# Performance work log

Hardware: AMD Instinct MI355X
Metric: run time of the kernel (lower is better)

The kernel has to match this reference:

```python
import jax, jax.numpy as jnp
import numpy as np

B, S, E, H, D, W = 2, 4096, 512, 8, 64, 512
NUM_BUCKETS, MAX_DISTANCE = 32, 128  # hardcoded in get_relative_positions for 't5'
NEG_INF = -1e30


def _t5_bucket_causal(relative_position):
    """T5 relative position bucketing, unidirectional (causal)."""
    n = jnp.maximum(-relative_position, 0)
    max_exact = NUM_BUCKETS // 2
    is_small = n < max_exact
    nf = jnp.maximum(n.astype(jnp.float32), 1.0)
    val_if_large = max_exact + (
        jnp.log(nf / max_exact) / np.log(MAX_DISTANCE / max_exact)
        * (NUM_BUCKETS - max_exact)
    ).astype(jnp.int32)
    val_if_large = jnp.minimum(val_if_large, NUM_BUCKETS - 1)
    return jnp.where(is_small, n, val_if_large)


def setup_inputs() -> dict:
    key = jax.random.key(0)
    ks = jax.random.split(key, 7)
    scale = 1.0 / np.sqrt(E)  # keep logits in a sane range
    return {
        'xs': jax.random.normal(ks[0], (B, S, E), jnp.float32),
        'prev_k': jax.random.normal(ks[1], (B, W, H, D), jnp.float32),
        'prev_v': jax.random.normal(ks[2], (B, W, H, D), jnp.float32),
        'w_q': jax.random.normal(ks[3], (E, H, D), jnp.float32) * scale,
        'w_k': jax.random.normal(ks[4], (E, H, D), jnp.float32) * scale,
        'w_v': jax.random.normal(ks[5], (E, H, D), jnp.float32) * scale,
        'rel_bias': jax.random.normal(ks[6], (H, NUM_BUCKETS), jnp.float32),
    }


def reference(xs, prev_k, prev_v, w_q, w_k, w_v, rel_bias):
    nw = S // W  # number of windows
    # kvq projections; queries pre-scaled by 1/sqrt(head_size)
    q = jnp.einsum('bse,ehd->bshd', xs, w_q) * (1.0 / np.sqrt(D))
    k = jnp.einsum('bse,ehd->bshd', xs, w_k)
    v = jnp.einsum('bse,ehd->bshd', xs, w_v)
    qw = q.reshape(B, nw, W, H, D)
    kw = k.reshape(B, nw, W, H, D)
    vw = v.reshape(B, nw, W, H, D)
    # Transformer-XL sliding window: keys for window i = [window i-1 keys ; window i keys]
    k_prev = jnp.concatenate([prev_k[:, None], kw[:, :-1]], axis=1)  # (B,nw,W,H,D)
    v_prev = jnp.concatenate([prev_v[:, None], vw[:, :-1]], axis=1)
    k2 = jnp.concatenate([k_prev, kw], axis=2)  # (B,nw,2W,H,D)
    v2 = jnp.concatenate([v_prev, vw], axis=2)
    # T5 relative position bias and causal mask (num_queries=W, num_keys=2W)
    ctx = jnp.arange(W)[:, None] + W          # query absolute position in key frame
    mem = jnp.arange(2 * W)[None, :]
    relpos = mem - ctx                        # (W, 2W), key - query
    bias = rel_bias[:, _t5_bucket_causal(relpos)]  # (H, W, 2W)
    # causal + window mask: key j attends iff i < j <= i+W (each query sees exactly W keys)
    mask = (relpos <= 0) & (relpos > -W)
    # attention per window
    scores = jnp.einsum('bnqhd,bnkhd->bnhqk', qw, k2)  # (B,nw,H,W,2W)
    scores = scores + bias[None, None]
    scores = jnp.where(mask[None, None, None], scores, NEG_INF)
    probs = jax.nn.softmax(scores, axis=-1)
    attn = jnp.einsum('bnhqk,bnkhd->bnqhd', probs, v2)
    attn_ys = attn.reshape(B, S, H, D)
    # next_kvi cache = last window's keys/values
    next_k = kw[:, -1]
    next_v = vw[:, -1]
    return attn_ys, next_k, next_v
```

## Files before the change

### kernel.cpp

```cpp
#include <hip/hip_runtime.h>
#include <hip/hip_bf16.h>
#include <math.h>

#define B_ 2
#define S_ 4096
#define E_ 512
#define H_ 8
#define D_ 64
#define W_ 512
#define NW_ 8

#define MASKV -1e30f
#define MINIT -1e4f

typedef float f32x4 __attribute__((ext_vector_type(4)));
typedef short s16x4 __attribute__((ext_vector_type(4)));
typedef short s16x8 __attribute__((ext_vector_type(8)));
typedef unsigned int u32;
typedef __attribute__((address_space(1))) const u32 as1_u32;
typedef __attribute__((address_space(3))) u32 as3_u32;

__device__ inline short f2bf(float f) {
    unsigned u = __builtin_bit_cast(unsigned, f);
    unsigned r = (u + 0x7FFFu + ((u >> 16) & 1u)) >> 16;
    return (short)r;
}
__device__ inline s16x8 pack8(f32x4 a, f32x4 b) {
    s16x8 r;
    r[0]=f2bf(a[0]); r[1]=f2bf(a[1]); r[2]=f2bf(a[2]); r[3]=f2bf(a[3]);
    r[4]=f2bf(b[0]); r[5]=f2bf(b[1]); r[6]=f2bf(b[2]); r[7]=f2bf(b[3]);
    return r;
}
__device__ __forceinline__ void gl_lds16(const void* g, void* l) {
    __builtin_amdgcn_global_load_lds((as1_u32*)(unsigned long long)g,
                                     (as3_u32*)(u32)(unsigned long long)l,
                                     16, 0, 0);
}

__global__ void convert_kernel(const float* __restrict__ xs, const float* __restrict__ pk,
                               const float* __restrict__ pv, short* __restrict__ xsbf,
                               short* __restrict__ pkbf, short* __restrict__ pvbf)
{
    size_t i8 = ((size_t)blockIdx.x * 256 + threadIdx.x) * 8;
    const float* src; short* dst; size_t off;
    if (i8 < 4194304)            { src = xs; dst = xsbf; off = i8; }
    else if (i8 < 4194304+524288){ src = pk; dst = pkbf; off = i8 - 4194304; }
    else                         { src = pv; dst = pvbf; off = i8 - 4194304 - 524288; }
    f32x4 a = *(const f32x4*)(src + off);
    f32x4 b = *(const f32x4*)(src + off + 4);
    *(s16x8*)(dst + off) = pack8(a, b);
}

__global__ void transpose_w_kernel(const float* __restrict__ wq, const float* __restrict__ wk,
                                   const float* __restrict__ wv, short* __restrict__ wt)
{
    __shared__ float st[64][68];
    const int k0 = blockIdx.x * 64;
    const int nt = blockIdx.y;
    const int z  = nt >> 3;
    const int n0 = (nt & 7) * 64;
    const float* wz = (z == 0) ? wq : (z == 1) ? wk : wv;
    const float scale = (z == 0) ? 0.125f : 1.0f;
    const int tid = threadIdx.x;
    {
        int kk = tid >> 4, nn = (tid & 15) * 4;
        #pragma unroll
        for (int it = 0; it < 4; ++it) {
            f32x4 x = *(const f32x4*)(wz + (size_t)(k0 + kk + it * 16) * 512 + n0 + nn);
            *(f32x4*)&st[kk + it * 16][nn] = x;
        }
    }
    __syncthreads();
    {
        int nn2 = tid >> 2, kseg = (tid & 3) * 16;
        s16x8 o0, o1;
        #pragma unroll
        for (int j = 0; j < 8; ++j) o0[j] = f2bf(st[kseg + j][nn2] * scale);
        #pragma unroll
        for (int j = 0; j < 8; ++j) o1[j] = f2bf(st[kseg + 8 + j][nn2] * scale);
        short* dst = wt + (size_t)(z * 512 + n0 + nn2) * 512 + k0 + kseg;
        *(s16x8*)(dst) = o0;
        *(s16x8*)(dst + 8) = o1;
    }
}

__global__ __launch_bounds__(256, 4)
void proj_kernel(const short* __restrict__ xsbf, const short* __restrict__ wt,
                 short* __restrict__ qkvbf, float* __restrict__ out)
{
    __shared__ short Xs[128][64];
    __shared__ short Ws[128][64];

    const int tid = threadIdx.x;
    const int m0  = blockIdx.x * 128;
    const int n0  = blockIdx.y * 128;
    const int z   = n0 >> 9;
    const int ln0 = n0 & 511;
    const int wave = tid >> 6, lane = tid & 63;
    const int wq = (wave & 1) * 64;
    const int wx = (wave >> 1) * 64;
    const int lr = lane & 15, quad = lane >> 4;

    f32x4 acc[4][4] = {};

    const int r8  = lane >> 3;
    const int gr  = lane & 7;

    for (int k0 = 0; k0 < 512; k0 += 64) {
        #pragma unroll
        for (int i = 0; i < 4; ++i) {
            int row = 32 * wave + 8 * i + r8;
            int gs  = gr ^ (row & 7);
            gl_lds16(xsbf + (size_t)(m0 + row) * 512 + k0 + gs * 8, &Xs[32 * wave + 8 * i][0]);
            gl_lds16(wt   + (size_t)(n0 + row) * 512 + k0 + gs * 8, &Ws[32 * wave + 8 * i][0]);
        }
        __syncthreads();
        #pragma unroll
        for (int ks = 0; ks < 2; ++ks) {
            s16x8 af[4], bf[4];
            #pragma unroll
            for (int ta = 0; ta < 4; ++ta) {
                int R = wq + ta * 16 + lr;
                af[ta] = *(const s16x8*)&Ws[R][(((ks * 4 + quad) ^ (R & 7)) * 8)];
            }
            #pragma unroll
            for (int tb = 0; tb < 4; ++tb) {
                int R = wx + tb * 16 + lr;
                bf[tb] = *(const s16x8*)&Xs[R][(((ks * 4 + quad) ^ (R & 7)) * 8)];
            }
            #pragma unroll
            for (int ta = 0; ta < 4; ++ta)
                #pragma unroll
                for (int tb = 0; tb < 4; ++tb)
                    acc[ta][tb] = __builtin_amdgcn_mfma_f32_16x16x32_bf16(
                        af[ta], bf[tb], acc[ta][tb], 0, 0, 0);
        }
        __syncthreads();
    }

    short* base = qkvbf + (size_t)z * ((size_t)8192 * 512);
    #pragma unroll
    for (int ta = 0; ta < 4; ++ta)
        #pragma unroll
        for (int tb = 0; tb < 4; ++tb) {
            int m  = m0 + wx + tb * 16 + lr;
            int ln = ln0 + wq + ta * 16 + quad * 4;
            s16x4 o;
            o[0] = f2bf(acc[ta][tb][0]); o[1] = f2bf(acc[ta][tb][1]);
            o[2] = f2bf(acc[ta][tb][2]); o[3] = f2bf(acc[ta][tb][3]);
            *(s16x4*)(base + (size_t)m * 512 + ln) = o;
            if (z != 0 && (m & 4095) >= 3584) {
                int bb = m >> 12, rr = (m & 4095) - 3584;
                float* dst = out + 4194304 + (size_t)(z - 1) * 524288
                           + ((size_t)(bb * 512 + rr)) * 512 + ln;
                *(f32x4*)dst = acc[ta][tb];
            }
        }
}

__global__ __launch_bounds__(256, 2)
void attn_kernel(const short* __restrict__ qkvbf, const short* __restrict__ pkbf,
                 const short* __restrict__ pvbf, const float* __restrict__ rel_bias,
                 float* __restrict__ out)
{
    __shared__ short qp_s[128][72];
    __shared__ short k_s[2][64][72];
    __shared__ short vt_s[2][64][72];
    __shared__ float bias_s[512];

    const short* qb = qkvbf;
    const short* kb = qkvbf + (size_t)8192 * 512;
    const short* vb = qkvbf + (size_t)2 * 8192 * 512;

    const int bid = blockIdx.x;
    const int qt = bid & 3;
    const int h  = (bid >> 2) & 7;
    const int n  = (bid >> 5) & 7;
    const int b  = bid >> 8;
    const int tid = threadIdx.x;
    const int wave = tid >> 6, lane = tid & 63;
    const int lr = lane & 15, quad = lane >> 4;
    const int q0 = qt * 128;
    const int i0 = q0 + 32 * wave;

    for (int nd = tid; nd < 512; nd += 256) {
        int bucket;
        if (nd < 16) bucket = nd;
        else {
            int vbk = 16 + (int)(log((double)nd * (1.0 / 16.0)) * (16.0 / log(8.0)));
            bucket = vbk < 31 ? vbk : 31;
        }
        bias_s[nd] = rel_bias[h * 32 + bucket];
    }

    {
        int row = tid >> 1, cs = (tid & 1) * 32;
        const short* src = qb + (size_t)(b * S_ + n * W_ + q0 + row) * 512 + h * 64 + cs;
        *(s16x8*)&qp_s[row][cs]      = *(const s16x8*)(src);
        *(s16x8*)&qp_s[row][cs + 8]  = *(const s16x8*)(src + 8);
        *(s16x8*)&qp_s[row][cs + 16] = *(const s16x8*)(src + 16);
        *(s16x8*)&qp_s[row][cs + 24] = *(const s16x8*)(src + 24);
    }
    s16x8 aq[2][2];
    #pragma unroll
    for (int tm = 0; tm < 2; ++tm)
        #pragma unroll
        for (int ks = 0; ks < 2; ++ks)
            aq[tm][ks] = *(const s16x8*)&qp_s[32 * wave + tm * 16 + lr][ks * 32 + quad * 8];

    f32x4 oacc[2][4] = {};
    float m_r[2][4], l_r[2][4];
    #pragma unroll
    for (int tm = 0; tm < 2; ++tm)
        #pragma unroll
        for (int rg = 0; rg < 4; ++rg) { m_r[tm][rg] = MINIT; l_r[tm][rg] = 0.f; }

    const int cmin = wave >> 1;
    const int cmax = 8 + (wave >> 1);

    const int ksr = tid >> 2;
    const int ksd = (tid & 3) * 16;
    const int vkey = tid & 63;
    const int vd0 = (tid >> 6) * 16;

    s16x8 rk0, rk1, rv0, rv1;
    {
        int jj = q0 + ksr;
        int p  = n * W_ + jj - W_;
        const short* ks = (p >= 0) ? kb + (size_t)(b * S_ + p) * 512 + h * 64 + ksd
                                   : pkbf + ((size_t)(b * W_ + jj) * H_ + h) * D_ + ksd;
        rk0 = *(const s16x8*)ks; rk1 = *(const s16x8*)(ks + 8);
        int jv = q0 + vkey;
        int pv = n * W_ + jv - W_;
        const short* vs = (pv >= 0) ? vb + (size_t)(b * S_ + pv) * 512 + h * 64 + vd0
                                    : pvbf + ((size_t)(b * W_ + jv) * H_ + h) * D_ + vd0;
        rv0 = *(const s16x8*)vs; rv1 = *(const s16x8*)(vs + 8);
    }

    for (int c = 0; c < 10; ++c) {
        const int pb = c & 1;
        *(s16x8*)&k_s[pb][ksr][ksd]     = rk0;
        *(s16x8*)&k_s[pb][ksr][ksd + 8] = rk1;
        #pragma unroll
        for (int m = 0; m < 8; ++m) vt_s[pb][vd0 + m][vkey] = rv0[m];
        #pragma unroll
        for (int m = 0; m < 8; ++m) vt_s[pb][vd0 + 8 + m][vkey] = rv1[m];

        {
            int cn = (c < 9) ? c + 1 : 9;
            int jj = q0 + 64 * cn + ksr;
            int p  = n * W_ + jj - W_;
            const short* ks = (p >= 0) ? kb + (size_t)(b * S_ + p) * 512 + h * 64 + ksd
                                       : pkbf + ((size_t)(b * W_ + jj) * H_ + h) * D_ + ksd;
            rk0 = *(const s16x8*)ks; rk1 = *(const s16x8*)(ks + 8);
            int jv = q0 + 64 * cn + vkey;
            int pv = n * W_ + jv - W_;
            const short* vs = (pv >= 0) ? vb + (size_t)(b * S_ + pv) * 512 + h * 64 + vd0
                                        : pvbf + ((size_t)(b * W_ + jv) * H_ + h) * D_ + vd0;
            rv0 = *(const s16x8*)vs; rv1 = *(const s16x8*)(vs + 8);
        }

        __syncthreads();
        if (c < cmin || c > cmax) continue;

        f32x4 sacc[2][4] = {};
        #pragma unroll
        for (int ks = 0; ks < 2; ++ks) {
            s16x8 bk[4];
            #pragma unroll
            for (int tn = 0; tn < 4; ++tn)
                bk[tn] = *(const s16x8*)&k_s[pb][tn * 16 + lr][ks * 32 + quad * 8];
            #pragma unroll
            for (int tm = 0; tm < 2; ++tm)
                #pragma unroll
                for (int tn = 0; tn < 4; ++tn)
                    sacc[tm][tn] = __builtin_amdgcn_mfma_f32_16x16x32_bf16(
                        aq[tm][ks], bk[tn], sacc[tm][tn], 0, 0, 0);
        }

        const int jc = q0 + 64 * c + lr;
        #pragma unroll
        for (int tm = 0; tm < 2; ++tm)
            #pragma unroll
            for (int tn = 0; tn < 4; ++tn) {
                int j = jc + tn * 16;
                #pragma unroll
                for (int rg = 0; rg < 4; ++rg) {
                    int i = i0 + tm * 16 + quad * 4 + rg;
                    unsigned dm1 = (unsigned)(j - i - 1);
                    int nd = (i + 512 - j) & 511;
                    float sv = sacc[tm][tn][rg] + bias_s[nd];
                    sacc[tm][tn][rg] = (dm1 < 512u) ? sv : MASKV;
                }
            }

        float rmax[2][4];
        #pragma unroll
        for (int tm = 0; tm < 2; ++tm)
            #pragma unroll
            for (int rg = 0; rg < 4; ++rg)
                rmax[tm][rg] = fmaxf(fmaxf(sacc[tm][0][rg], sacc[tm][1][rg]),
                                     fmaxf(sacc[tm][2][rg], sacc[tm][3][rg]));
        #pragma unroll
        for (int off = 1; off < 16; off <<= 1)
            #pragma unroll
            for (int tm = 0; tm < 2; ++tm)
                #pragma unroll
                for (int rg = 0; rg < 4; ++rg)
                    rmax[tm][rg] = fmaxf(rmax[tm][rg], __shfl_xor(rmax[tm][rg], off));

        float al[2][4], rs[2][4];
        #pragma unroll
        for (int tm = 0; tm < 2; ++tm)
            #pragma unroll
            for (int rg = 0; rg < 4; ++rg) {
                float mo = m_r[tm][rg];
                float mn = fmaxf(mo, rmax[tm][rg]);
                al[tm][rg] = __expf(mo - mn);
                m_r[tm][rg] = mn;
                rs[tm][rg] = 0.f;
            }

        #pragma unroll
        for (int tm = 0; tm < 2; ++tm)
            #pragma unroll
            for (int tn = 0; tn < 4; ++tn)
                #pragma unroll
                for (int rg = 0; rg < 4; ++rg) {
                    float p = __expf(sacc[tm][tn][rg] - m_r[tm][rg]);
                    rs[tm][rg] += p;
                    qp_s[32 * wave + tm * 16 + quad * 4 + rg][tn * 16 + lr] = f2bf(p);
                }

        #pragma unroll
        for (int off = 1; off < 16; off <<= 1)
            #pragma unroll
            for (int tm = 0; tm < 2; ++tm)
                #pragma unroll
                for (int rg = 0; rg < 4; ++rg)
                    rs[tm][rg] += __shfl_xor(rs[tm][rg], off);

        #pragma unroll
        for (int tm = 0; tm < 2; ++tm)
            #pragma unroll
            for (int rg = 0; rg < 4; ++rg)
                l_r[tm][rg] = l_r[tm][rg] * al[tm][rg] + rs[tm][rg];

        #pragma unroll
        for (int tm = 0; tm < 2; ++tm)
            #pragma unroll
            for (int tn = 0; tn < 4; ++tn)
                #pragma unroll
                for (int rg = 0; rg < 4; ++rg)
                    oacc[tm][tn][rg] *= al[tm][rg];

        asm volatile("s_waitcnt lgkmcnt(0)" ::: "memory");

        #pragma unroll
        for (int ks = 0; ks < 2; ++ks) {
            s16x8 ap[2], bv[4];
            #pragma unroll
            for (int tm = 0; tm < 2; ++tm)
                ap[tm] = *(const s16x8*)&qp_s[32 * wave + tm * 16 + lr][ks * 32 + quad * 8];
            #pragma unroll
            for (int tn = 0; tn < 4; ++tn)
                bv[tn] = *(const s16x8*)&vt_s[pb][tn * 16 + lr][ks * 32 + quad * 8];
            #pragma unroll
            for (int tm = 0; tm < 2; ++tm)
                #pragma unroll
                for (int tn = 0; tn < 4; ++tn)
                    oacc[tm][tn] = __builtin_amdgcn_mfma_f32_16x16x32_bf16(
                        ap[tm], bv[tn], oacc[tm][tn], 0, 0, 0);
        }
    }

    #pragma unroll
    for (int tm = 0; tm < 2; ++tm)
        #pragma unroll
        for (int rg = 0; rg < 4; ++rg) {
            int row = i0 + tm * 16 + quad * 4 + rg;
            float linv = 1.0f / l_r[tm][rg];
            float* dst = out + (((size_t)b * S_ + n * W_ + row) * H_ + h) * D_ + lr;
            #pragma unroll
            for (int tn = 0; tn < 4; ++tn)
                dst[tn * 16] = oacc[tm][tn][rg] * linv;
        }
}

extern "C" void kernel_launch(void* const* d_in, const int* in_sizes, int n_in,
                              void* d_out, int out_size, void* d_ws, size_t ws_size,
                              hipStream_t stream)
{
    const float* xs       = (const float*)d_in[0];
    const float* prev_k   = (const float*)d_in[1];
    const float* prev_v   = (const float*)d_in[2];
    const float* w_q      = (const float*)d_in[3];
    const float* w_k      = (const float*)d_in[4];
    const float* w_v      = (const float*)d_in[5];
    const float* rel_bias = (const float*)d_in[6];
    float* out = (float*)d_out;

    short* xsbf  = (short*)d_ws;
    short* wt    = xsbf + (size_t)8192 * 512;
    short* qkvbf = wt + (size_t)1536 * 512;
    short* pkbf  = qkvbf + (size_t)3 * 8192 * 512;
    short* pvbf  = pkbf + (size_t)524288;

    convert_kernel<<<2560, 256, 0, stream>>>(xs, prev_k, prev_v, xsbf, pkbf, pvbf);
    transpose_w_kernel<<<dim3(8, 24), 256, 0, stream>>>(w_q, w_k, w_v, wt);

    proj_kernel<<<dim3(64, 12), 256, 0, stream>>>(xsbf, wt, qkvbf, out);

    attn_kernel<<<512, 256, 0, stream>>>(qkvbf, pkbf, pvbf, rel_bias, out);
}
```

Measured before the change: 150.8 us.

## Split attention block into eight waves of 16 query rows each

The attention kernel moves from 4 waves handling 32 query rows each to 8 waves handling 16 rows each, with 512 threads per block. K/V tile loading is spread over twice as many threads, and Q is loaded straight from global memory into registers instead of being staged through shared memory. Each wave now skips more fully masked key chunks, and the added waves should improve latency hiding, at the cost of reusing each K/V fragment read from LDS over fewer MFMAs and more per-block synchronisation overhead.

```diff
diff --git a/kernel.cpp b/kernel.cpp
--- a/kernel.cpp
+++ b/kernel.cpp
@@ -158,12 +158,12 @@
         }
 }
 
-__global__ __launch_bounds__(256, 2)
+__global__ __launch_bounds__(512, 4)
 void attn_kernel(const short* __restrict__ qkvbf, const short* __restrict__ pkbf,
                  const short* __restrict__ pvbf, const float* __restrict__ rel_bias,
                  float* __restrict__ out)
 {
-    __shared__ short qp_s[128][72];
+    __shared__ short p_s[128][72];
     __shared__ short k_s[2][64][72];
     __shared__ short vt_s[2][64][72];
     __shared__ float bias_s[512];
@@ -181,9 +181,10 @@
     const int wave = tid >> 6, lane = tid & 63;
     const int lr = lane & 15, quad = lane >> 4;
     const int q0 = qt * 128;
-    const int i0 = q0 + 32 * wave;
-
-    for (int nd = tid; nd < 512; nd += 256) {
+    const int i0 = q0 + 16 * wave;
+
+    {
+        int nd = tid;
         int bucket;
         if (nd < 16) bucket = nd;
         else {
@@ -193,58 +194,45 @@
         bias_s[nd] = rel_bias[h * 32 + bucket];
     }
 
-    {
-        int row = tid >> 1, cs = (tid & 1) * 32;
-        const short* src = qb + (size_t)(b * S_ + n * W_ + q0 + row) * 512 + h * 64 + cs;
-        *(s16x8*)&qp_s[row][cs]      = *(const s16x8*)(src);
-        *(s16x8*)&qp_s[row][cs + 8]  = *(const s16x8*)(src + 8);
-        *(s16x8*)&qp_s[row][cs + 16] = *(const s16x8*)(src + 16);
-        *(s16x8*)&qp_s[row][cs + 24] = *(const s16x8*)(src + 24);
-    }
-    s16x8 aq[2][2];
+    s16x8 aq[2];
+    {
+        const short* src = qb + (size_t)(b * S_ + n * W_ + i0 + lr) * 512 + h * 64 + quad * 8;
+        aq[0] = *(const s16x8*)(src);
+        aq[1] = *(const s16x8*)(src + 32);
+    }
+
+    f32x4 oacc[4] = {};
+    float m_r[4], l_r[4];
     #pragma unroll
-    for (int tm = 0; tm < 2; ++tm)
-        #pragma unroll
-        for (int ks = 0; ks < 2; ++ks)
-            aq[tm][ks] = *(const s16x8*)&qp_s[32 * wave + tm * 16 + lr][ks * 32 + quad * 8];
-
-    f32x4 oacc[2][4] = {};
-    float m_r[2][4], l_r[2][4];
-    #pragma unroll
-    for (int tm = 0; tm < 2; ++tm)
-        #pragma unroll
-        for (int rg = 0; rg < 4; ++rg) { m_r[tm][rg] = MINIT; l_r[tm][rg] = 0.f; }
-
-    const int cmin = wave >> 1;
-    const int cmax = 8 + (wave >> 1);
-
-    const int ksr = tid >> 2;
-    const int ksd = (tid & 3) * 16;
+    for (int rg = 0; rg < 4; ++rg) { m_r[rg] = MINIT; l_r[rg] = 0.f; }
+
+    const int cmin = (16 * wave) >> 6;
+    int cmax = (16 * wave + 528) >> 6; if (cmax > 9) cmax = 9;
+
+    const int ksr = tid >> 3;
+    const int ksd = (tid & 7) * 8;
     const int vkey = tid & 63;
-    const int vd0 = (tid >> 6) * 16;
-
-    s16x8 rk0, rk1, rv0, rv1;
+    const int vd0 = (tid >> 6) * 8;
+
+    s16x8 rk, rv;
     {
         int jj = q0 + ksr;
         int p  = n * W_ + jj - W_;
         const short* ks = (p >= 0) ? kb + (size_t)(b * S_ + p) * 512 + h * 64 + ksd
                                    : pkbf + ((size_t)(b * W_ + jj) * H_ + h) * D_ + ksd;
-        rk0 = *(const s16x8*)ks; rk1 = *(const s16x8*)(ks + 8);
+        rk = *(const s16x8*)ks;
         int jv = q0 + vkey;
         int pv = n * W_ + jv - W_;
         const short* vs = (pv >= 0) ? vb + (size_t)(b * S_ + pv) * 512 + h * 64 + vd0
                                     : pvbf + ((size_t)(b * W_ + jv) * H_ + h) * D_ + vd0;
-        rv0 = *(const s16x8*)vs; rv1 = *(const s16x8*)(vs + 8);
+        rv = *(const s16x8*)vs;
     }
 
     for (int c = 0; c < 10; ++c) {
         const int pb = c & 1;
-        *(s16x8*)&k_s[pb][ksr][ksd]     = rk0;
-        *(s16x8*)&k_s[pb][ksr][ksd + 8] = rk1;
-        #pragma unroll
-        for (int m = 0; m < 8; ++m) vt_s[pb][vd0 + m][vkey] = rv0[m];
-        #pragma unroll
-        for (int m = 0; m < 8; ++m) vt_s[pb][vd0 + 8 + m][vkey] = rv1[m];
+        *(s16x8*)&k_s[pb][ksr][ksd] = rk;
+        #pragma unroll
+        for (int m = 0; m < 8; ++m) vt_s[pb][vd0 + m][vkey] = rv[m];
 
         {
             int cn = (c < 9) ? c + 1 : 9;
@@ -252,18 +240,18 @@
             int p  = n * W_ + jj - W_;
             const short* ks = (p >= 0) ? kb + (size_t)(b * S_ + p) * 512 + h * 64 + ksd
                                        : pkbf + ((size_t)(b * W_ + jj) * H_ + h) * D_ + ksd;
-            rk0 = *(const s16x8*)ks; rk1 = *(const s16x8*)(ks + 8);
+            rk = *(const s16x8*)ks;
             int jv = q0 + 64 * cn + vkey;
             int pv = n * W_ + jv - W_;
             const short* vs = (pv >= 0) ? vb + (size_t)(b * S_ + pv) * 512 + h * 64 + vd0
                                         : pvbf + ((size_t)(b * W_ + jv) * H_ + h) * D_ + vd0;
-            rv0 = *(const s16x8*)vs; rv1 = *(const s16x8*)(vs + 8);
+            rv = *(const s16x8*)vs;
         }
 
         __syncthreads();
         if (c < cmin || c > cmax) continue;
 
-        f32x4 sacc[2][4] = {};
+        f32x4 sacc[4] = {};
         #pragma unroll
         for (int ks = 0; ks < 2; ++ks) {
             s16x8 bk[4];
@@ -271,120 +259,96 @@
             for (int tn = 0; tn < 4; ++tn)
                 bk[tn] = *(const s16x8*)&k_s[pb][tn * 16 + lr][ks * 32 + quad * 8];
             #pragma unroll
-            for (int tm = 0; tm < 2; ++tm)
-                #pragma unroll
-                for (int tn = 0; tn < 4; ++tn)
-                    sacc[tm][tn] = __builtin_amdgcn_mfma_f32_16x16x32_bf16(
-                        aq[tm][ks], bk[tn], sacc[tm][tn], 0, 0, 0);
+            for (int tn = 0; tn < 4; ++tn)
+                sacc[tn] = __builtin_amdgcn_mfma_f32_16x16x32_bf16(
+                    aq[ks], bk[tn], sacc[tn], 0, 0, 0);
         }
 
         const int jc = q0 + 64 * c + lr;
         #pragma unroll
-        for (int tm = 0; tm < 2; ++tm)
-            #pragma unroll
-            for (int tn = 0; tn < 4; ++tn) {
-                int j = jc + tn * 16;
-                #pragma unroll
-                for (int rg = 0; rg < 4; ++rg) {
-                    int i = i0 + tm * 16 + quad * 4 + rg;
-                    unsigned dm1 = (unsigned)(j - i - 1);
-                    int nd = (i + 512 - j) & 511;
-                    float sv = sacc[tm][tn][rg] + bias_s[nd];
-                    sacc[tm][tn][rg] = (dm1 < 512u) ? sv : MASKV;
-                }
-            }
-
-        float rmax[2][4];
-        #pragma unroll
-        for (int tm = 0; tm < 2; ++tm)
+        for (int tn = 0; tn < 4; ++tn) {
+            int j = jc + tn * 16;
+            #pragma unroll
+            for (int rg = 0; rg < 4; ++rg) {
+                int i = i0 + quad * 4 + rg;
+                unsigned dm1 = (unsigned)(j - i - 1);
+                int nd = (i + 512 - j) & 511;
+                float sv = sacc[tn][rg] + bias_s[nd];
+                sacc[tn][rg] = (dm1 < 512u) ? sv : MASKV;
+            }
+        }
+
+        float rmax[4];
+        #pragma unroll
+        for (int rg = 0; rg < 4; ++rg)
+            rmax[rg] = fmaxf(fmaxf(sacc[0][rg], sacc[1][rg]),
+                             fmaxf(sacc[2][rg], sacc[3][rg]));
+        #pragma unroll
+        for (int off = 1; off < 16; off <<= 1)
             #pragma unroll
             for (int rg = 0; rg < 4; ++rg)
-                rmax[tm][rg] = fmaxf(fmaxf(sacc[tm][0][rg], sacc[tm][1][rg]),
-                                     fmaxf(sacc[tm][2][rg], sacc[tm][3][rg]));
+                rmax[rg] = fmaxf(rmax[rg], __shfl_xor(rmax[rg], off));
+
+        float al[4], rs[4];
+        #pragma unroll
+        for (int rg = 0; rg < 4; ++rg) {
+            float mo = m_r[rg];
+            float mn = fmaxf(mo, rmax[rg]);
+            al[rg] = __expf(mo - mn);
+            m_r[rg] = mn;
+            rs[rg] = 0.f;
+        }
+
+        #pragma unroll
+        for (int tn = 0; tn < 4; ++tn)
+            #pragma unroll
+            for (int rg = 0; rg < 4; ++rg) {
+                float p = __expf(sacc[tn][rg] - m_r[rg]);
+                rs[rg] += p;
+                p_s[16 * wave + quad * 4 + rg][tn * 16 + lr] = f2bf(p);
+            }
+
         #pragma unroll
         for (int off = 1; off < 16; off <<= 1)
             #pragma unroll
-            for (int tm = 0; tm < 2; ++tm)
-                #pragma unroll
-                for (int rg = 0; rg < 4; ++rg)
-                    rmax[tm][rg] = fmaxf(rmax[tm][rg], __shfl_xor(rmax[tm][rg], off));
-
-        float al[2][4], rs[2][4];
-        #pragma unroll
-        for (int tm = 0; tm < 2; ++tm)
-            #pragma unroll
-            for (int rg = 0; rg < 4; ++rg) {
-                float mo = m_r[tm][rg];
-                float mn = fmaxf(mo, rmax[tm][rg]);
-                al[tm][rg] = __expf(mo - mn);
-                m_r[tm][rg] = mn;
-                rs[tm][rg] = 0.f;
-            }
-
-        #pragma unroll
-        for (int tm = 0; tm < 2; ++tm)
-            #pragma unroll
-            for (int tn = 0; tn < 4; ++tn)
-                #pragma unroll
-                for (int rg = 0; rg < 4; ++rg) {
-                    float p = __expf(sacc[tm][tn][rg] - m_r[tm][rg]);
-                    rs[tm][rg] += p;
-                    qp_s[32 * wave + tm * 16 + quad * 4 + rg][tn * 16 + lr] = f2bf(p);
-                }
-
-        #pragma unroll
-        for (int off = 1; off < 16; off <<= 1)
-            #pragma unroll
-            for (int tm = 0; tm < 2; ++tm)
-                #pragma unroll
-                for (int rg = 0; rg < 4; ++rg)
-                    rs[tm][rg] += __shfl_xor(rs[tm][rg], off);
-
-        #pragma unroll
-        for (int tm = 0; tm < 2; ++tm)
-            #pragma unroll
             for (int rg = 0; rg < 4; ++rg)
-                l_r[tm][rg] = l_r[tm][rg] * al[tm][rg] + rs[tm][rg];
-
-        #pragma unroll
-        for (int tm = 0; tm < 2; ++tm)
-            #pragma unroll
-            for (int tn = 0; tn < 4; ++tn)
-                #pragma unroll
-                for (int rg = 0; rg < 4; ++rg)
-                    oacc[tm][tn][rg] *= al[tm][rg];
+                rs[rg] += __shfl_xor(rs[rg], off);
+
+        #pragma unroll
+        for (int rg = 0; rg < 4; ++rg)
+            l_r[rg] = l_r[rg] * al[rg] + rs[rg];
+
+        #pragma unroll
+        for (int tn = 0; tn < 4; ++tn)
+            #pragma unroll
+            for (int rg = 0; rg < 4; ++rg)
+                oacc[tn][rg] *= al[rg];
 
         asm volatile("s_waitcnt lgkmcnt(0)" ::: "memory");
 
         #pragma unroll
         for (int ks = 0; ks < 2; ++ks) {
-            s16x8 ap[2], bv[4];
-            #pragma unroll
-            for (int tm = 0; tm < 2; ++tm)
-                ap[tm] = *(const s16x8*)&qp_s[32 * wave + tm * 16 + lr][ks * 32 + quad * 8];
+            s16x8 ap = *(const s16x8*)&p_s[16 * wave + lr][ks * 32 + quad * 8];
+            s16x8 bv[4];
             #pragma unroll
             for (int tn = 0; tn < 4; ++tn)
                 bv[tn] = *(const s16x8*)&vt_s[pb][tn * 16 + lr][ks * 32 + quad * 8];
             #pragma unroll
-            for (int tm = 0; tm < 2; ++tm)
-                #pragma unroll
-                for (int tn = 0; tn < 4; ++tn)
-                    oacc[tm][tn] = __builtin_amdgcn_mfma_f32_16x16x32_bf16(
-                        ap[tm], bv[tn], oacc[tm][tn], 0, 0, 0);
+            for (int tn = 0; tn < 4; ++tn)
+                oacc[tn] = __builtin_amdgcn_mfma_f32_16x16x32_bf16(
+                    ap, bv[tn], oacc[tn], 0, 0, 0);
         }
     }
 
     #pragma unroll
-    for (int tm = 0; tm < 2; ++tm)
-        #pragma unroll
-        for (int rg = 0; rg < 4; ++rg) {
-            int row = i0 + tm * 16 + quad * 4 + rg;
-            float linv = 1.0f / l_r[tm][rg];
-            float* dst = out + (((size_t)b * S_ + n * W_ + row) * H_ + h) * D_ + lr;
-            #pragma unroll
-            for (int tn = 0; tn < 4; ++tn)
-                dst[tn * 16] = oacc[tm][tn][rg] * linv;
-        }
+    for (int rg = 0; rg < 4; ++rg) {
+        int row = i0 + quad * 4 + rg;
+        float linv = 1.0f / l_r[rg];
+        float* dst = out + (((size_t)b * S_ + n * W_ + row) * H_ + h) * D_ + lr;
+        #pragma unroll
+        for (int tn = 0; tn < 4; ++tn)
+            dst[tn * 16] = oacc[tn][rg] * linv;
+    }
 }
 
 extern "C" void kernel_launch(void* const* d_in, const int* in_sizes, int n_in,
@@ -411,5 +375,5 @@
 
     proj_kernel<<<dim3(64, 12), 256, 0, stream>>>(xsbf, wt, qkvbf, out);
 
-    attn_kernel<<<512, 256, 0, stream>>>(qkvbf, pkbf, pvbf, rel_bias, out);
-}
+    attn_kernel<<<512, 512, 0, stream>>>(qkvbf, pkbf, pvbf, rel_bias, out);
+}
```

Result: faster. 146.8 us (-2.6%).
